# Kernel optimization log

Measured on AMD Instinct MI355X. Metric: run time of the kernel, lower is better.

The kernel has to match this reference:

```python
import jax, jax.numpy as jnp
import numpy as np

LMAX = 4  # number of l blocks (lmax+1 in the original)
# segment ids mapping the L2 = sum(2l+1) = 16 spherical components to their l block
SEG = np.repeat(np.arange(LMAX), 2 * np.arange(LMAX) + 1)  # [16]
SEG_ONEHOT = np.eye(LMAX, dtype=np.float32)[SEG]  # [16, LMAX]


def setup_inputs() -> dict:
    key = jax.random.key(0)
    ks = jax.random.split(key, 10)
    b, m, f, k, L2 = 16, 64, 128, 64, 16
    def rnd(kk, shape, scale):
        return jax.random.normal(kk, shape, dtype=jnp.float32) * scale
    return {
        'x': rnd(ks[0], (b, m, f, L2), 1.0),
        'y': rnd(ks[1], (b, m, f, L2), 1.0),
        'wx0': rnd(ks[2], (k, f, f, LMAX), 1.0 / np.sqrt(f * f * LMAX)),
        'wy0': rnd(ks[3], (k, f, f, LMAX), 1.0 / np.sqrt(f * f * LMAX)),
        'wx_mlp': rnd(ks[4], (2, k, k), 1.0 / np.sqrt(k)),
        'bx_mlp': rnd(ks[5], (2, k, k), 0.02),
        'wy_mlp': rnd(ks[6], (2, k, k), 1.0 / np.sqrt(k)),
        'by_mlp': rnd(ks[7], (2, k, k), 0.02),
        'wxf': rnd(ks[8], (LMAX, f, k), 1.0 / np.sqrt(k)),
        'wyf': rnd(ks[9], (LMAX, f, k), 1.0 / np.sqrt(k)),
    }


def reference(x, y, wx0, wy0, wx_mlp, bx_mlp, wy_mlp, by_mlp, wxf, wyf):
    act = jax.nn.silu
    S = jnp.asarray(SEG_ONEHOT)  # [L2, lmax]
    # outer product of y and x features, segment-summed over each l block:
    # mix[b,m,fy,fx,l] = sum_c y[b,m,fy,c] * x[b,m,fx,c] * S[c,l]
    mix = jnp.einsum('bmfc,bmgc,cl->bmfgl', y, x, S)  # [b,m,f,f,lmax]
    mx = jnp.einsum('bmfgl,kfgl->bmk', mix, wx0)
    my = jnp.einsum('bmfgl,kfgl->bmk', mix, wy0)
    for i in range(wx_mlp.shape[0]):  # the n_mlp-1 used MLP stages
        mx = act(jnp.einsum('bmk,kl->bml', mx, wx_mlp[i]) + bx_mlp[i])
        my = act(jnp.einsum('bmk,kl->bml', my, wy_mlp[i]) + by_mlp[i])
    mx = act(jnp.einsum('bmk,lfk->bmfl', mx, wxf))  # [b,m,f,lmax]
    my = act(jnp.einsum('bmk,lfk->bmfl', my, wyf))
    # broadcast each l gate over its 2l+1 components (repeat == gather by SEG)
    seg = jnp.asarray(SEG)
    res = mx[..., seg] * x + my[..., seg] * y  # [b,m,f,L2]
    return res
```

## Files before the change

### kernel.cpp

```cpp
#include <hip/hip_runtime.h>
#include <stdint.h>


#define AS1 __attribute__((address_space(1)))
#define AS3 __attribute__((address_space(3)))

typedef __bf16 bf16x8 __attribute__((ext_vector_type(8)));
typedef float f32x4 __attribute__((ext_vector_type(4)));

__device__ __forceinline__ uint16_t f2b(float f) {
  uint32_t u = __float_as_uint(f);
  u += 0x7fffu + ((u >> 16) & 1u);
  return (uint16_t)(u >> 16);
}

#if __has_builtin(__builtin_amdgcn_fdot2_f32_bf16)
typedef __bf16 bf16x2 __attribute__((ext_vector_type(2)));
__device__ __forceinline__ float dot2b(uint32_t a, uint32_t b, float c) {
  union { uint32_t u; bf16x2 v; } ua, ub;
  ua.u = a; ub.u = b;
  return __builtin_amdgcn_fdot2_f32_bf16(ua.v, ub.v, c, false);
}
#else
__device__ __forceinline__ float dot2b(uint32_t a, uint32_t b, float c) {
  float a0 = __uint_as_float(a << 16), a1 = __uint_as_float(a & 0xffff0000u);
  float b0 = __uint_as_float(b << 16), b1 = __uint_as_float(b & 0xffff0000u);
  return c + a0 * b0 + a1 * b1;
}
#endif

__global__ __launch_bounds__(256) void convert_all(
    const float* __restrict__ wx0, const float* __restrict__ wy0,
    const float* __restrict__ x, const float* __restrict__ y,
    const float* __restrict__ wxf, const float* __restrict__ wyf,
    uint16_t* __restrict__ Wb2, uint16_t* __restrict__ xb,
    uint16_t* __restrict__ yb, float* __restrict__ wfT) {
  int bid = blockIdx.x, tid = threadIdx.x;
  if (bid < 4096) {
    int c = bid * 256 + tid;
    int fb = c >> 16;
    int rem = c & 65535;
    int fy = rem >> 9;
    int rem2 = rem & 511;
    int n = rem2 >> 2, pos = rem2 & 3;
    int slot = pos ^ ((n >> 1) & 3);
    int k = n & 63;
    const float* src = (n < 64 ? wx0 : wy0) +
        ((size_t)(k * 128 + fy) * 512 + fb * 32 + slot * 8);
    float4 v0 = *(const float4*)src;
    float4 v1 = *(const float4*)(src + 4);
    uint32_t o0 = (uint32_t)f2b(v0.x) | ((uint32_t)f2b(v0.y) << 16);
    uint32_t o1 = (uint32_t)f2b(v0.z) | ((uint32_t)f2b(v0.w) << 16);
    uint32_t o2 = (uint32_t)f2b(v1.x) | ((uint32_t)f2b(v1.y) << 16);
    uint32_t o3 = (uint32_t)f2b(v1.z) | ((uint32_t)f2b(v1.w) << 16);
    *(uint4*)(Wb2 + (size_t)c * 8) = make_uint4(o0, o1, o2, o3);
    return;
  }
  if (bid >= 6144) {
    int base = (bid - 6144) * 2048 + tid * 8;
#pragma unroll
    for (int ii = 0; ii < 8; ++ii) {
      int idx = base + ii;
      int side = idx >> 15, rem = idx & 32767;
      int k = rem >> 9, l = (rem >> 7) & 3, f = rem & 127;
      const float* src = side ? wyf : wxf;
      wfT[idx] = src[((size_t)l * 128 + f) * 64 + k];
    }
    return;
  }
  size_t i = ((size_t)(bid - 4096) * 256 + tid) * 8;
  const float* s; uint16_t* d;
  if (i < 2097152) { s = x + i;             d = xb + i; }
  else             { s = y + (i - 2097152); d = yb + (i - 2097152); }
  float4 v0 = *(const float4*)s;
  float4 v1 = *(const float4*)(s + 4);
  uint32_t o0 = (uint32_t)f2b(v0.x) | ((uint32_t)f2b(v0.y) << 16);
  uint32_t o1 = (uint32_t)f2b(v0.z) | ((uint32_t)f2b(v0.w) << 16);
  uint32_t o2 = (uint32_t)f2b(v1.x) | ((uint32_t)f2b(v1.y) << 16);
  uint32_t o3 = (uint32_t)f2b(v1.z) | ((uint32_t)f2b(v1.w) << 16);
  *(uint4*)d = make_uint4(o0, o1, o2, o3);
}

__device__ __forceinline__ void gload_lds16(const void* g, void* l) {
  __builtin_amdgcn_global_load_lds((const AS1 uint32_t*)g, (AS3 uint32_t*)l, 16, 0, 0);
}

#define PIPE_BAR(N) \
  asm volatile("s_waitcnt vmcnt(" #N ") lgkmcnt(0)\n\ts_barrier" ::: "memory")

__global__ __launch_bounds__(512, 4) void fused_gemm(
    const uint16_t* __restrict__ xb, const uint16_t* __restrict__ yb,
    const uint16_t* __restrict__ Wb2, float* __restrict__ Cpart) {
  __shared__ __align__(16) uint16_t sA[2][128 * 32];
  __shared__ __align__(16) uint16_t sB[3][128 * 32];
  __shared__ __align__(16) uint16_t yS[3][2048];

  int tid = threadIdx.x;
  int w = tid >> 6, lane = tid & 63;
  int g_id = blockIdx.x;
  int fb = g_id >> 2, fyg = g_id & 3;
  int FB = fb * 8;
  int fy0 = fyg * 32;
  int m0 = blockIdx.y * 128;
  int r = lane & 15, q = lane >> 4;
  int wm = w >> 2, wn = w & 3;
  int m_loc = tid & 127, quarter = tid >> 7;

  uint32_t xr[16];
  {
    const uint16_t* xp0 = xb + (size_t)(m0 + m_loc) * 2048 + (FB + quarter * 2) * 16;
#pragma unroll
    for (int j = 0; j < 4; ++j) {
      uint4 v = *(const uint4*)(xp0 + j * 8);
      xr[j * 4 + 0] = v.x; xr[j * 4 + 1] = v.y;
      xr[j * 4 + 2] = v.z; xr[j * 4 + 3] = v.w;
    }
  }

  f32x4 zero = {0.f, 0.f, 0.f, 0.f};
  f32x4 acc[4][2];
#pragma unroll
  for (int i = 0; i < 4; ++i)
#pragma unroll
    for (int j = 0; j < 2; ++j) acc[i][j] = zero;

  auto issueB = [&](uint16_t* dstB, int t) {
    if (w < 4) {
      size_t base = (size_t)(fb * 128 + fy0 + t) * 4096;
#pragma unroll
      for (int jj = 0; jj < 2; ++jj) {
        int blk = w * 2 + jj;
        gload_lds16(Wb2 + base + blk * 512 + lane * 8, dstB + blk * 512);
      }
    }
  };
  int ychunk = (w >> 1) & 1, ymbase = (w & 1) * 64;
  const uint16_t* ysrc_base = yb + (size_t)(m0 + ymbase + lane) * 2048 + ychunk * 8;
  int ydst_off = ychunk * 1024 + ymbase * 8;
  auto issueY = [&](uint16_t* dstY, int t) {
    if (w >= 4) gload_lds16(ysrc_base + (size_t)(fy0 + t) * 16, dstY + ydst_off);
  };

  auto computeG = [&](const uint16_t* srcY, float* gg) {
    uint4 ya = *(const uint4*)(srcY + m_loc * 8);
    uint4 yc = *(const uint4*)(srcY + 1024 + m_loc * 8);
    uint32_t yp[8] = {ya.x, ya.y, ya.z, ya.w, yc.x, yc.y, yc.z, yc.w};
    uint32_t yl0 = yp[0] & 0xffffu, yh0 = yp[0] & 0xffff0000u;
    uint32_t yl4 = yp[4] & 0xffffu, yh4 = yp[4] & 0xffff0000u;
#pragma unroll
    for (int fxp = 0; fxp < 2; ++fxp) {
      const uint32_t* xp = xr + fxp * 8;
      gg[fxp * 4 + 0] = dot2b(xp[0], yl0, 0.f);
      gg[fxp * 4 + 1] = dot2b(xp[1], yp[1], dot2b(xp[0], yh0, 0.f));
      gg[fxp * 4 + 2] = dot2b(xp[4], yl4,
                         dot2b(xp[3], yp[3], dot2b(xp[2], yp[2], 0.f)));
      gg[fxp * 4 + 3] = dot2b(xp[7], yp[7], dot2b(xp[6], yp[6],
                         dot2b(xp[5], yp[5], dot2b(xp[4], yh4, 0.f))));
    }
  };
  auto writeA = [&](uint16_t* dstA, const float* gg) {
    uint32_t o[4];
#pragma unroll
    for (int p = 0; p < 4; ++p)
      o[p] = (__float_as_uint(gg[2 * p]) >> 16) |
             (__float_as_uint(gg[2 * p + 1]) & 0xffff0000u);
    int pos = quarter ^ ((m_loc >> 1) & 3);
    *(uint4*)(dstA + m_loc * 32 + pos * 8) = make_uint4(o[0], o[1], o[2], o[3]);
  };

  float gg[8];
  issueY(yS[0], 0);
  __syncthreads();
  computeG(yS[0], gg);
  writeA(sA[0], gg);
  issueB(sB[0], 0);
  issueY(yS[1], 1);
  issueB(sB[1], 1);
  issueY(yS[2], 2);
  if (w < 4) PIPE_BAR(2); else PIPE_BAR(1);

  uint16_t *pAc = sA[0], *pAn = sA[1];
  uint16_t *pBread = sB[0], *pBmid = sB[1], *pBissue = sB[2];
  uint16_t *pYcomp = yS[1], *pYmid = yS[2], *pYissue = yS[0];

  for (int t = 0; t < 32; ++t) {
    if (t <= 29) issueB(pBissue, t + 2);
    if (t <= 28) issueY(pYissue, t + 3);

    bf16x8 a[4], b[2];
#pragma unroll
    for (int i = 0; i < 4; ++i) {
      int row = wm * 64 + i * 16 + r;
      int pos = q ^ ((row >> 1) & 3);
      a[i] = *(const bf16x8*)&pAc[row * 32 + pos * 8];
    }
#pragma unroll
    for (int j = 0; j < 2; ++j) {
      int row = wn * 32 + j * 16 + r;
      int pos = q ^ ((row >> 1) & 3);
      b[j] = *(const bf16x8*)&pBread[row * 32 + pos * 8];
    }

    if (t < 31) {
      computeG(pYcomp, gg);
      writeA(pAn, gg);
    }

    __builtin_amdgcn_s_setprio(1);
#pragma unroll
    for (int i = 0; i < 4; ++i)
#pragma unroll
      for (int j = 0; j < 2; ++j)
        acc[i][j] = __builtin_amdgcn_mfma_f32_16x16x32_bf16(a[i], b[j], acc[i][j], 0, 0, 0);
    __builtin_amdgcn_s_setprio(0);

    if (t <= 28)      { if (w < 4) PIPE_BAR(2); else PIPE_BAR(1); }
    else if (t == 29) { if (w < 4) PIPE_BAR(2); else PIPE_BAR(0); }
    else if (t == 30) PIPE_BAR(0);

    uint16_t* tp;
    tp = pAc; pAc = pAn; pAn = tp;
    tp = pBread; pBread = pBmid; pBmid = pBissue; pBissue = tp;
    tp = pYcomp; pYcomp = pYmid; pYmid = pYissue; pYissue = tp;
  }

#pragma unroll
  for (int i = 0; i < 4; ++i)
#pragma unroll
    for (int j = 0; j < 2; ++j)
#pragma unroll
      for (int reg = 0; reg < 4; ++reg) {
        int mm = m0 + wm * 64 + i * 16 + q * 4 + reg;
        int nn = wn * 32 + j * 16 + r;
        Cpart[((size_t)mm * 64 + g_id) * 128 + nn] = acc[i][j][reg];
      }
}

__global__ __launch_bounds__(256) void finish_kernel(
    const float* __restrict__ x, const float* __restrict__ y,
    const float* __restrict__ wx_mlp, const float* __restrict__ bx_mlp,
    const float* __restrict__ wy_mlp, const float* __restrict__ by_mlp,
    const float* __restrict__ wfT,
    const float* __restrict__ Cpart, float* __restrict__ out) {
  const int seg[16] = {0,1,1,1,2,2,2,2,2,3,3,3,3,3,3,3};
  __shared__ float sred[256];
  __shared__ float sm[128];
  __shared__ float sg[2][128][4];
  int t = threadIdx.x;
  int bm = blockIdx.x;
  int mi = bm & 63;

  {
    int col = t & 127, hh = t >> 7;
    const float* cp = Cpart + ((size_t)bm * 64 + hh * 32) * 128 + col;
    float s = 0.f;
#pragma unroll 8
    for (int sp = 0; sp < 32; ++sp)
      s += cp[(size_t)sp * 128];
    sred[t] = s;
  }
  __syncthreads();
  if (t < 128) sm[t] = sred[t] + sred[t + 128];
  __syncthreads();

  for (int st = 0; st < 2; ++st) {
    float v = 0.f;
    if (t < 128) {
      int side = t >> 6, j = t & 63;
      const float* wmlp = side ? wy_mlp : wx_mlp;
      const float* bmlp = side ? by_mlp : bx_mlp;
      const float* mv = sm + side * 64;
#pragma unroll 8
      for (int k = 0; k < 64; ++k)
        v += mv[k] * wmlp[(st * 64 + k) * 64 + j];
      v += bmlp[(st * 64 + mi) * 64 + j];
      v = v / (1.f + __expf(-v));
    }
    __syncthreads();
    if (t < 128) sm[t] = v;
    __syncthreads();
  }

  {
    int side = t >> 7, f = t & 127;
    const float* base = wfT + side * 32768;
    const float* mv = sm + side * 64;
    float gg[4] = {0.f, 0.f, 0.f, 0.f};
#pragma unroll 8
    for (int k = 0; k < 64; ++k) {
      float m2 = mv[k];
#pragma unroll
      for (int l = 0; l < 4; ++l)
        gg[l] += m2 * base[(k * 4 + l) * 128 + f];
    }
#pragma unroll
    for (int l = 0; l < 4; ++l)
      sg[side][f][l] = gg[l] / (1.f + __expf(-gg[l]));
  }
  __syncthreads();

  {
    int f = t >> 1, half = t & 1;
    size_t base = ((size_t)bm * 128 + f) * 16 + half * 8;
    float4 xa = *(const float4*)(x + base), xb4 = *(const float4*)(x + base + 4);
    float4 ya = *(const float4*)(y + base), yb4 = *(const float4*)(y + base + 4);
    float xv[8] = {xa.x, xa.y, xa.z, xa.w, xb4.x, xb4.y, xb4.z, xb4.w};
    float yv[8] = {ya.x, ya.y, ya.z, ya.w, yb4.x, yb4.y, yb4.z, yb4.w};
    float o[8];
#pragma unroll
    for (int ii = 0; ii < 8; ++ii) {
      int c = half * 8 + ii;
      o[ii] = sg[0][f][seg[c]] * xv[ii] + sg[1][f][seg[c]] * yv[ii];
    }
    *(float4*)(out + base)     = make_float4(o[0], o[1], o[2], o[3]);
    *(float4*)(out + base + 4) = make_float4(o[4], o[5], o[6], o[7]);
  }
}

extern "C" void kernel_launch(void* const* d_in, const int* in_sizes, int n_in,
                              void* d_out, int out_size, void* d_ws, size_t ws_size,
                              hipStream_t stream) {
  const float* x      = (const float*)d_in[0];
  const float* y      = (const float*)d_in[1];
  const float* wx0    = (const float*)d_in[2];
  const float* wy0    = (const float*)d_in[3];
  const float* wx_mlp = (const float*)d_in[4];
  const float* bx_mlp = (const float*)d_in[5];
  const float* wy_mlp = (const float*)d_in[6];
  const float* by_mlp = (const float*)d_in[7];
  const float* wxf    = (const float*)d_in[8];
  const float* wyf    = (const float*)d_in[9];
  float* out = (float*)d_out;

  uint16_t* Wb2   = (uint16_t*)d_ws;
  uint16_t* xb    = (uint16_t*)((char*)d_ws + (size_t)16777216);
  uint16_t* yb    = (uint16_t*)((char*)d_ws + (size_t)20971520);
  float*    Cpart = (float*)((char*)d_ws + (size_t)25165824);
  float*    wfT   = (float*)((char*)d_ws + (size_t)58720256);

  convert_all<<<6176, 256, 0, stream>>>(wx0, wy0, x, y, wxf, wyf, Wb2, xb, yb, wfT);
  fused_gemm<<<dim3(64, 8), 512, 0, stream>>>(xb, yb, Wb2, Cpart);
  finish_kernel<<<1024, 256, 0, stream>>>(x, y, wx_mlp, bx_mlp, wy_mlp, by_mlp,
                                          wfT, Cpart, out);
}
```

Measured before the change: 166.1 us.

## Transpose y to fy-major bf16 and prefetch it into registers instead of LDS

The conversion kernel now writes y in an fy-major transposed bf16 layout, so each thread can read its 16 spherical components for a given fy with two contiguous 16-byte global loads. The gemm kernel drops the y LDS triple buffer and its async global-to-LDS loads. Instead it keeps a two-deep register prefetch of y, with the loop unrolled by two to alternate register sets, and adjusts the vmcnt waits to match. This frees LDS and removes the LDS round trip for y. In exchange it adds per-thread global loads that the waits must cover, plus scheduling barriers.

```diff
diff --git a/kernel.cpp b/kernel.cpp
--- a/kernel.cpp
+++ b/kernel.cpp
@@ -34,7 +34,7 @@
     const float* __restrict__ x, const float* __restrict__ y,
     const float* __restrict__ wxf, const float* __restrict__ wyf,
     uint16_t* __restrict__ Wb2, uint16_t* __restrict__ xb,
-    uint16_t* __restrict__ yb, float* __restrict__ wfT) {
+    uint16_t* __restrict__ ybT, float* __restrict__ wfT) {
   int bid = blockIdx.x, tid = threadIdx.x;
   if (bid < 4096) {
     int c = bid * 256 + tid;
@@ -68,32 +68,46 @@
     }
     return;
   }
-  size_t i = ((size_t)(bid - 4096) * 256 + tid) * 8;
-  const float* s; uint16_t* d;
-  if (i < 2097152) { s = x + i;             d = xb + i; }
-  else             { s = y + (i - 2097152); d = yb + (i - 2097152); }
-  float4 v0 = *(const float4*)s;
-  float4 v1 = *(const float4*)(s + 4);
-  uint32_t o0 = (uint32_t)f2b(v0.x) | ((uint32_t)f2b(v0.y) << 16);
-  uint32_t o1 = (uint32_t)f2b(v0.z) | ((uint32_t)f2b(v0.w) << 16);
-  uint32_t o2 = (uint32_t)f2b(v1.x) | ((uint32_t)f2b(v1.y) << 16);
-  uint32_t o3 = (uint32_t)f2b(v1.z) | ((uint32_t)f2b(v1.w) << 16);
-  *(uint4*)d = make_uint4(o0, o1, o2, o3);
+  if (bid < 5120) {
+    size_t i = ((size_t)(bid - 4096) * 256 + tid) * 8;
+    const float* s = x + i;
+    float4 v0 = *(const float4*)s;
+    float4 v1 = *(const float4*)(s + 4);
+    uint32_t o0 = (uint32_t)f2b(v0.x) | ((uint32_t)f2b(v0.y) << 16);
+    uint32_t o1 = (uint32_t)f2b(v0.z) | ((uint32_t)f2b(v0.w) << 16);
+    uint32_t o2 = (uint32_t)f2b(v1.x) | ((uint32_t)f2b(v1.y) << 16);
+    uint32_t o3 = (uint32_t)f2b(v1.z) | ((uint32_t)f2b(v1.w) << 16);
+    *(uint4*)(xb + i) = make_uint4(o0, o1, o2, o3);
+    return;
+  }
+  {
+    int c = (bid - 5120) * 256 + tid;
+    int half = c & 1, fy = (c >> 1) & 127, m = c >> 8;
+    const float* s = y + (size_t)c * 8;
+    float4 v0 = *(const float4*)s;
+    float4 v1 = *(const float4*)(s + 4);
+    uint32_t o0 = (uint32_t)f2b(v0.x) | ((uint32_t)f2b(v0.y) << 16);
+    uint32_t o1 = (uint32_t)f2b(v0.z) | ((uint32_t)f2b(v0.w) << 16);
+    uint32_t o2 = (uint32_t)f2b(v1.x) | ((uint32_t)f2b(v1.y) << 16);
+    uint32_t o3 = (uint32_t)f2b(v1.z) | ((uint32_t)f2b(v1.w) << 16);
+    *(uint4*)(ybT + ((size_t)fy * 1024 + m) * 16 + half * 8) =
+        make_uint4(o0, o1, o2, o3);
+  }
 }
 
 __device__ __forceinline__ void gload_lds16(const void* g, void* l) {
   __builtin_amdgcn_global_load_lds((const AS1 uint32_t*)g, (AS3 uint32_t*)l, 16, 0, 0);
 }
 
+#define SB0 __builtin_amdgcn_sched_barrier(0)
 #define PIPE_BAR(N) \
   asm volatile("s_waitcnt vmcnt(" #N ") lgkmcnt(0)\n\ts_barrier" ::: "memory")
 
 __global__ __launch_bounds__(512, 4) void fused_gemm(
-    const uint16_t* __restrict__ xb, const uint16_t* __restrict__ yb,
+    const uint16_t* __restrict__ xb, const uint16_t* __restrict__ ybT,
     const uint16_t* __restrict__ Wb2, float* __restrict__ Cpart) {
   __shared__ __align__(16) uint16_t sA[2][128 * 32];
   __shared__ __align__(16) uint16_t sB[3][128 * 32];
-  __shared__ __align__(16) uint16_t yS[3][2048];
 
   int tid = threadIdx.x;
   int w = tid >> 6, lane = tid & 63;
@@ -134,16 +148,10 @@
       }
     }
   };
-  int ychunk = (w >> 1) & 1, ymbase = (w & 1) * 64;
-  const uint16_t* ysrc_base = yb + (size_t)(m0 + ymbase + lane) * 2048 + ychunk * 8;
-  int ydst_off = ychunk * 1024 + ymbase * 8;
-  auto issueY = [&](uint16_t* dstY, int t) {
-    if (w >= 4) gload_lds16(ysrc_base + (size_t)(fy0 + t) * 16, dstY + ydst_off);
-  };
-
-  auto computeG = [&](const uint16_t* srcY, float* gg) {
-    uint4 ya = *(const uint4*)(srcY + m_loc * 8);
-    uint4 yc = *(const uint4*)(srcY + 1024 + m_loc * 8);
+
+  const uint16_t* ybase = ybT + (size_t)(m0 + m_loc) * 16;
+
+  auto computeG = [&](uint4 ya, uint4 yc, float* gg) {
     uint32_t yp[8] = {ya.x, ya.y, ya.z, ya.w, yc.x, yc.y, yc.z, yc.w};
     uint32_t yl0 = yp[0] & 0xffffu, yh0 = yp[0] & 0xffff0000u;
     uint32_t yl4 = yp[4] & 0xffffu, yh4 = yp[4] & 0xffff0000u;
@@ -168,25 +176,31 @@
     *(uint4*)(dstA + m_loc * 32 + pos * 8) = make_uint4(o[0], o[1], o[2], o[3]);
   };
 
-  float gg[8];
-  issueY(yS[0], 0);
-  __syncthreads();
-  computeG(yS[0], gg);
-  writeA(sA[0], gg);
-  issueB(sB[0], 0);
-  issueY(yS[1], 1);
-  issueB(sB[1], 1);
-  issueY(yS[2], 2);
-  if (w < 4) PIPE_BAR(2); else PIPE_BAR(1);
-
   uint16_t *pAc = sA[0], *pAn = sA[1];
   uint16_t *pBread = sB[0], *pBmid = sB[1], *pBissue = sB[2];
-  uint16_t *pYcomp = yS[1], *pYmid = yS[2], *pYissue = yS[0];
-
-  for (int t = 0; t < 32; ++t) {
+
+  float gg[8];
+  issueB(pBread, 0);
+  issueB(pBmid, 1);
+  SB0;
+  uint4 yev0, yev1, yod0, yod1;
+  {
+    const uint16_t* yp0 = ybase + (size_t)fy0 * 16384;
+    uint4 t0a = *(const uint4*)yp0;
+    uint4 t0b = *(const uint4*)(yp0 + 8);
+    computeG(t0a, t0b, gg);
+    writeA(pAc, gg);
+    yev0 = *(const uint4*)(ybase + (size_t)(fy0 + 1) * 16384);
+    yev1 = *(const uint4*)(ybase + (size_t)(fy0 + 1) * 16384 + 8);
+    yod0 = *(const uint4*)(ybase + (size_t)(fy0 + 2) * 16384);
+    yod1 = *(const uint4*)(ybase + (size_t)(fy0 + 2) * 16384 + 8);
+  }
+  SB0;
+  PIPE_BAR(4);
+
+  auto body = [&](int t, uint4& y0_, uint4& y1_) {
     if (t <= 29) issueB(pBissue, t + 2);
-    if (t <= 28) issueY(pYissue, t + 3);
-
+    SB0;
     bf16x8 a[4], b[2];
 #pragma unroll
     for (int i = 0; i < 4; ++i) {
@@ -200,12 +214,15 @@
       int pos = q ^ ((row >> 1) & 3);
       b[j] = *(const bf16x8*)&pBread[row * 32 + pos * 8];
     }
-
     if (t < 31) {
-      computeG(pYcomp, gg);
+      computeG(y0_, y1_, gg);
       writeA(pAn, gg);
     }
-
+    if (t <= 28) {
+      y0_ = *(const uint4*)(ybase + (size_t)(fy0 + t + 3) * 16384);
+      y1_ = *(const uint4*)(ybase + (size_t)(fy0 + t + 3) * 16384 + 8);
+    }
+    SB0;
     __builtin_amdgcn_s_setprio(1);
 #pragma unroll
     for (int i = 0; i < 4; ++i)
@@ -214,14 +231,18 @@
         acc[i][j] = __builtin_amdgcn_mfma_f32_16x16x32_bf16(a[i], b[j], acc[i][j], 0, 0, 0);
     __builtin_amdgcn_s_setprio(0);
 
-    if (t <= 28)      { if (w < 4) PIPE_BAR(2); else PIPE_BAR(1); }
-    else if (t == 29) { if (w < 4) PIPE_BAR(2); else PIPE_BAR(0); }
+    if (t <= 28)      { if (w < 4) PIPE_BAR(6); else PIPE_BAR(4); }
+    else if (t == 29) { if (w < 4) PIPE_BAR(4); else PIPE_BAR(4); }
     else if (t == 30) PIPE_BAR(0);
 
     uint16_t* tp;
     tp = pAc; pAc = pAn; pAn = tp;
     tp = pBread; pBread = pBmid; pBmid = pBissue; pBissue = tp;
-    tp = pYcomp; pYcomp = pYmid; pYmid = pYissue; pYissue = tp;
+  };
+
+  for (int t = 0; t < 32; t += 2) {
+    body(t, yev0, yev1);
+    body(t + 1, yod0, yod1);
   }
 
 #pragma unroll
@@ -334,12 +355,12 @@
 
   uint16_t* Wb2   = (uint16_t*)d_ws;
   uint16_t* xb    = (uint16_t*)((char*)d_ws + (size_t)16777216);
-  uint16_t* yb    = (uint16_t*)((char*)d_ws + (size_t)20971520);
+  uint16_t* ybT   = (uint16_t*)((char*)d_ws + (size_t)20971520);
   float*    Cpart = (float*)((char*)d_ws + (size_t)25165824);
   float*    wfT   = (float*)((char*)d_ws + (size_t)58720256);
 
-  convert_all<<<6176, 256, 0, stream>>>(wx0, wy0, x, y, wxf, wyf, Wb2, xb, yb, wfT);
-  fused_gemm<<<dim3(64, 8), 512, 0, stream>>>(xb, yb, Wb2, Cpart);
+  convert_all<<<6176, 256, 0, stream>>>(wx0, wy0, x, y, wxf, wyf, Wb2, xb, ybT, wfT);
+  fused_gemm<<<dim3(64, 8), 512, 0, stream>>>(xb, ybT, Wb2, Cpart);
   finish_kernel<<<1024, 256, 0, stream>>>(x, y, wx_mlp, bx_mlp, wy_mlp, by_mlp,
                                           wfT, Cpart, out);
 }
```

Result: faster. 162.8 us (-2.0%).
